# Kernel tuning notes

Measured on AMD Instinct MI355X. Metric: run time of the kernel, lower is better.

## Reference

```python
import jax, jax.numpy as jnp
import numpy as np

B, N, NE = 2, 100000, 800000
S, F, D = 3, 2, 128          # space_size, n_fields, enc_dim
TD, CD, SD = 11, 32, 10      # enc_t_dim, cond_dim, spatial_dim


def _mlp(x, w1, b1, w2, b2):
    # Linear -> SiLU -> Linear (MLP with n_hidden=1, hidden=128, no layernorm)
    return jax.nn.silu(x @ w1 + b1) @ w2 + b2


def setup_inputs() -> dict:
    key = jax.random.key(0)
    ks = iter(jax.random.split(key, 40))

    def w(shape):
        fan_in = shape[-2] if len(shape) >= 2 else shape[-1]
        return jax.random.normal(next(ks), shape, jnp.float32) / np.sqrt(fan_in)

    def b(shape):
        return jnp.zeros(shape, jnp.float32)

    inp = dict(
        node_pos=jax.random.normal(next(ks), (B, N, S), jnp.float32),
        state_in=jax.random.normal(next(ks), (B, N, F), jnp.float32),
        time_i=jax.random.normal(next(ks), (B, TD), jnp.float32),
        conditions=jax.random.normal(next(ks), (B, CD), jnp.float32),
        spatial_inform=jax.random.normal(next(ks), (B, SD), jnp.float32),
        edges=jax.random.randint(next(ks), (B, NE, 2), 0, N, jnp.int64)
        if jax.config.jax_enable_x64 else jax.random.randint(next(ks), (B, NE, 2), 0, N, jnp.int32),
        # per-field node MLPs, stacked over fields: input = space_size + 1
        fields_w1=w((F, S + 1, D)), fields_b1=b((F, D)),
        fields_w2=w((F, D, D)), fields_b2=b((F, D)),
        # time / cond / spatial MLPs
        time_w1=w((TD, D)), time_b1=b((D,)), time_w2=w((D, D)), time_b2=b((D,)),
        cond_w1=w((CD, D)), cond_b1=b((D,)), cond_w2=w((D, D)), cond_b2=b((D,)),
        spat_w1=w((SD, D)), spat_b1=b((D,)), spat_w2=w((D, D)), spat_b2=b((D,)),
        # fuse_para: 3*D -> 128 -> 2*D
        fuse_w1=w((3 * D, D)), fuse_b1=b((D,)),
        fuse_w2=w((D, 2 * D)), fuse_b2=b((2 * D,)),
        # edge MLP: 2*S+1 -> 128 -> D
        fe_w1=w((2 * S + 1, D)), fe_b1=b((D,)),
        fe_w2=w((D, D)), fe_b2=b((D,)),
    )
    return inp


def reference(node_pos, state_in, time_i, conditions, spatial_inform, edges,
              fields_w1, fields_b1, fields_w2, fields_b2,
              time_w1, time_b1, time_w2, time_b2,
              cond_w1, cond_b1, cond_w2, cond_b2,
              spat_w1, spat_b1, spat_w2, spat_b2,
              fuse_w1, fuse_b1, fuse_w2, fuse_b2,
              fe_w1, fe_b1, fe_w2, fe_b2):
    # FiLM parameters from time + condition + spatial encodings
    time_enc = _mlp(time_i, time_w1, time_b1, time_w2, time_b2)        # [B,D]
    cond_enc = _mlp(conditions, cond_w1, cond_b1, cond_w2, cond_b2)    # [B,D]
    spat_enc = _mlp(spatial_inform, spat_w1, spat_b1, spat_w2, spat_b2)
    h = jnp.concatenate([cond_enc, time_enc, spat_enc], axis=-1)       # [B,3D]
    para = _mlp(h, fuse_w1, fuse_b1, fuse_w2, fuse_b2)                 # [B,2D]
    gamma, beta = jnp.split(para, 2, axis=-1)                          # [B,D] each

    # Per-field node MLPs, vectorized over fields: x_f [B,N,F,S+1]
    pos_b = jnp.broadcast_to(node_pos[:, :, None, :], (node_pos.shape[0], node_pos.shape[1], F, S))
    x_f = jnp.concatenate([pos_b, state_in[..., None]], axis=-1)       # [B,N,F,S+1]
    hid = jax.nn.silu(jnp.einsum('bnfd,fde->bnfe', x_f, fields_w1) + fields_b1)
    V = jnp.einsum('bnfe,feo->bnfo', hid, fields_w2) + fields_b2       # [B,N,F,D]
    V = V * gamma[:, None, None, :] + beta[:, None, None, :]

    # Edge features: gather sender/receiver positions, diff/norm/concat
    idx_s = jnp.broadcast_to(edges[..., 0:1], edges.shape[:2] + (S,))
    idx_r = jnp.broadcast_to(edges[..., 1:2], edges.shape[:2] + (S,))
    senders = jnp.take_along_axis(node_pos, idx_s, axis=1)             # [B,NE,S]
    receivers = jnp.take_along_axis(node_pos, idx_r, axis=1)
    d = receivers - senders
    norm = jnp.sqrt(jnp.sum(d * d, axis=-1, keepdims=True) + 1e-8)
    e_feat = jnp.concatenate([d, -d, norm], axis=-1)                   # [B,NE,2S+1]
    E = _mlp(e_feat, fe_w1, fe_b1, fe_w2, fe_b2)                       # [B,NE,D]

    return V, E
```

## Files before the change

### kernel.cpp

```cpp
#include <hip/hip_runtime.h>
#include <hip/hip_bf16.h>
#include <string.h>

#define B_  2
#define N_  100000
#define NE_ 800000
#define F_  2
#define D_  128
#define TD_ 11
#define CD_ 32
#define SD_ 10

#define NODE_BX   782
#define NODE_NB   (NODE_BX * F_ * B_)
#define EDGE_BX   6250
#define EDGE_NB   (EDGE_BX * B_)
#define GROUPS    3125
#define TOTAL_NB  (NODE_NB + EDGE_NB)

#define WS_GB      0
#define WS_FLAG    2048
#define WS_W1PACK  2112
#define WS_W2FRAG  14400

typedef short s16x8 __attribute__((ext_vector_type(8)));
typedef float f32x4 __attribute__((ext_vector_type(4)));
typedef unsigned u32x4 __attribute__((ext_vector_type(4)));

static __device__ __forceinline__ unsigned short f2bf(float f) {
    unsigned u = __builtin_bit_cast(unsigned, f);
    u += 0x7FFFu + ((u >> 16) & 1u);
    return (unsigned short)(u >> 16);
}
static __device__ __forceinline__ float silu_f(float x) {
    return x * __builtin_amdgcn_rcpf(1.0f + __expf(-x));
}
static __device__ __forceinline__ unsigned pack_bf16(float lo, float hi) {
    __hip_bfloat162 c = __float22bfloat162_rn(make_float2(lo, hi));
    unsigned r;
    memcpy(&r, &c, sizeof(r));
    return r;
}
static __device__ __forceinline__ void lds_barrier() {
    asm volatile("s_waitcnt lgkmcnt(0)" ::: "memory");
    __builtin_amdgcn_s_barrier();
}

__global__ void prep_kernel(
    const float* __restrict__ time_i, const float* __restrict__ cond,
    const float* __restrict__ spat,
    const float* tw1, const float* tb1, const float* tw2, const float* tb2,
    const float* cw1, const float* cb1, const float* cw2, const float* cb2,
    const float* sw1, const float* sb1, const float* sw2, const float* sb2,
    const float* fuw1, const float* fub1, const float* fuw2, const float* fub2,
    const float* __restrict__ fw1, const float* __restrict__ fb1,
    const float* __restrict__ fw2,
    const float* __restrict__ ew1, const float* __restrict__ eb1,
    const float* __restrict__ ew2,
    const int* __restrict__ edges,
    char* __restrict__ ws)
{
    const int bx = blockIdx.x, t = threadIdx.x;

    if (bx < 2) {
        const int b = bx, d = t;
        __shared__ float h[3 * D_];
        __shared__ float hid[D_];

        const float* X [3] = { cond + b * CD_, time_i + b * TD_, spat + b * SD_ };
        const float* W1[3] = { cw1, tw1, sw1 };
        const float* B1[3] = { cb1, tb1, sb1 };
        const float* W2[3] = { cw2, tw2, sw2 };
        const float* B2[3] = { cb2, tb2, sb2 };
        const int    K [3] = { CD_, TD_, SD_ };

        for (int m = 0; m < 3; ++m) {
            float a = 0.f;
            if (d < D_) {
                a = B1[m][d];
                for (int k = 0; k < K[m]; ++k) a += X[m][k] * W1[m][k * D_ + d];
            }
            __syncthreads();
            if (d < D_) hid[d] = a / (1.0f + __expf(-a));
            __syncthreads();
            if (d < D_) {
                float o = B2[m][d];
                for (int k = 0; k < D_; ++k) o += hid[k] * W2[m][k * D_ + d];
                h[m * D_ + d] = o;
            }
        }
        __syncthreads();
        float pre2 = 0.f;
        if (d < D_) {
            pre2 = fub1[d];
            for (int k = 0; k < 3 * D_; ++k) pre2 += h[k] * fuw1[k * D_ + d];
        }
        __syncthreads();
        if (d < D_) hid[d] = pre2 / (1.0f + __expf(-pre2));
        __syncthreads();
        if (d < D_) {
            float g = fub2[d], be = fub2[D_ + d];
            for (int k = 0; k < D_; ++k) {
                float hv = hid[k];
                g  += hv * fuw2[k * 2 * D_ + d];
                be += hv * fuw2[k * 2 * D_ + D_ + d];
            }
            float* gb = (float*)ws;
            gb[(b * 2 + 0) * D_ + d] = g;
            gb[(b * 2 + 1) * D_ + d] = be;
        }
    } else if (bx < 5) {
        const int which = bx - 2;
        const float* src = (which < 2) ? (fw2 + which * D_ * D_) : ew2;
        unsigned short* dst = (unsigned short*)(ws + WS_W2FRAG) + (long)which * 2048 * 8;
        for (int e = t; e < 2048; e += 256) {
            const int lanee = e & 63, kb = (e >> 6) & 3, nt = e >> 8;
            const int out = nt * 16 + (lanee & 15);
            const int k0  = kb * 32 + (lanee >> 4) * 8;
            s16x8 v;
            #pragma unroll
            for (int i = 0; i < 8; ++i)
                v[i] = (short)f2bf(src[(k0 + i) * D_ + out]);
            *(s16x8*)(dst + e * 8) = v;
        }
    } else {
        float* w1p = (float*)(ws + WS_W1PACK);
        if (t == 0) {
            int nz = 0;
            for (int j = 0; j < 64; ++j) nz |= edges[2 * j + 1];
            ((float*)(ws + WS_FLAG))[0] = (nz == 0) ? 1.0f : 0.0f;
        }
        {
            const int f = t >> 7, e = t & 127;
            float* dst = w1p + (f * 128 + e) * 8;
            #pragma unroll
            for (int k = 0; k < 4; ++k) dst[k] = fw1[(f * 4 + k) * D_ + e];
            dst[4] = fb1[f * D_ + e];
            dst[5] = 0.f; dst[6] = 0.f; dst[7] = 0.f;
        }
        if (t < 128) {
            const int e = t;
            float* dst = w1p + (2 * 128 + e) * 8;
            dst[0] = ew1[0 * D_ + e] - ew1[3 * D_ + e];
            dst[1] = ew1[1 * D_ + e] - ew1[4 * D_ + e];
            dst[2] = ew1[2 * D_ + e] - ew1[5 * D_ + e];
            dst[3] = ew1[6 * D_ + e];
            dst[4] = eb1[e];
            dst[5] = 0.f; dst[6] = 0.f; dst[7] = 0.f;
        }
    }
}

__global__ __launch_bounds__(256, 4) void fused_kernel(
    const float* __restrict__ pos, const float* __restrict__ state,
    const int* __restrict__ edges,
    const float* __restrict__ fb2, const float* __restrict__ eb2,
    const char* __restrict__ ws,
    float* __restrict__ V, float* __restrict__ E)
{
    __shared__ __align__(16) char smem[34816];
    unsigned short* w2lds = (unsigned short*)smem;
    float*          outF  = (float*)smem;

    const int bx = blockIdx.x, t = threadIdx.x;
    const int lane = t & 63, wv = t >> 6;
    const int kg = lane >> 4, lr = lane & 15;

    const float* gbAll = (const float*)ws;
    const float* w1all = (const float*)(ws + WS_W1PACK);
    const unsigned short* w2all = (const unsigned short*)(ws + WS_W2FRAG);

    bool isNode; int sub;
    if (bx >= 5 * GROUPS) { isNode = true; sub = GROUPS + (bx - 5 * GROUPS); }
    else {
        int g = bx / 5, s = bx - 5 * g;
        if (s == 0) { isNode = true;  sub = g; }
        else        { isNode = false; sub = g * 4 + (s - 1); }
    }

    float xa[4], xb[4];
    int n0 = 0, f = 0, b, e0blk = 0;
    if (isNode) {
        n0 = (sub % NODE_BX) * 128;
        f  = (sub / NODE_BX) & 1;
        b  = sub / (NODE_BX * F_);
        int na = n0 + wv * 32 + lr;      if (na >= N_) na = N_ - 1;
        int nb = n0 + wv * 32 + lr + 16; if (nb >= N_) nb = N_ - 1;
        long pa = ((long)b * N_ + na) * 3, pb = ((long)b * N_ + nb) * 3;
        xa[0] = pos[pa]; xa[1] = pos[pa + 1]; xa[2] = pos[pa + 2];
        xb[0] = pos[pb]; xb[1] = pos[pb + 1]; xb[2] = pos[pb + 2];
        xa[3] = state[((long)b * N_ + na) * F_ + f];
        xb[3] = state[((long)b * N_ + nb) * F_ + f];
    } else {
        e0blk = (sub % EDGE_BX) * 128;
        b     = sub / EDGE_BX;
        const bool x64 = ((const float*)(ws + WS_FLAG))[0] > 0.5f;
        const long ea = (long)b * NE_ + e0blk + wv * 32 + lr;
        const long eb = ea + 16;
        int sa, ra, sb, rb;
        if (x64) {
            sa = edges[ea * 4]; ra = edges[ea * 4 + 2];
            sb = edges[eb * 4]; rb = edges[eb * 4 + 2];
        } else {
            int2 va = *(const int2*)(edges + ea * 2); sa = va.x; ra = va.y;
            int2 vb = *(const int2*)(edges + eb * 2); sb = vb.x; rb = vb.y;
        }
        const float* pp = pos + (long)b * N_ * 3;
        {
            long so = (long)sa * 3, ro = (long)ra * 3;
            xa[0] = pp[ro]     - pp[so];
            xa[1] = pp[ro + 1] - pp[so + 1];
            xa[2] = pp[ro + 2] - pp[so + 2];
            xa[3] = sqrtf(xa[0]*xa[0] + xa[1]*xa[1] + xa[2]*xa[2] + 1e-8f);
        }
        {
            long so = (long)sb * 3, ro = (long)rb * 3;
            xb[0] = pp[ro]     - pp[so];
            xb[1] = pp[ro + 1] - pp[so + 1];
            xb[2] = pp[ro + 2] - pp[so + 2];
            xb[3] = sqrtf(xb[0]*xb[0] + xb[1]*xb[1] + xb[2]*xb[2] + 1e-8f);
        }
    }

    const int which = isNode ? f : 2;
    {
        const char* src = (const char*)(w2all + (long)which * 2048 * 8);
        #pragma unroll
        for (int j = 0; j < 8; ++j) {
            f32x4 v = *(const f32x4*)(src + (j * 256 + t) * 16);
            *(f32x4*)((char*)w2lds + (j * 256 + t) * 16) = v;
        }
    }
    __syncthreads();

    const float* w1g = w1all + which * 1024;

    f32x4 acc[2][8];
    #pragma unroll
    for (int mt = 0; mt < 2; ++mt)
        #pragma unroll
        for (int nt = 0; nt < 8; ++nt) acc[mt][nt] = (f32x4){0.f, 0.f, 0.f, 0.f};

    #pragma unroll
    for (int kb = 0; kb < 4; ++kb) {
        const int e0 = kb * 32 + kg * 8;
        u32x4 da, db;
        #pragma unroll
        for (int j = 0; j < 4; ++j) {
            const float* wp0 = w1g + (e0 + 2 * j) * 8;
            const float* wp1 = wp0 + 8;
            f32x4 wA = *(const f32x4*)wp0;  const float bbA = wp0[4];
            f32x4 wB = *(const f32x4*)wp1;  const float bbB = wp1[4];
            float pa0 = silu_f(xa[0]*wA[0] + xa[1]*wA[1] + xa[2]*wA[2] + xa[3]*wA[3] + bbA);
            float pa1 = silu_f(xa[0]*wB[0] + xa[1]*wB[1] + xa[2]*wB[2] + xa[3]*wB[3] + bbB);
            float pb0 = silu_f(xb[0]*wA[0] + xb[1]*wA[1] + xb[2]*wA[2] + xb[3]*wA[3] + bbA);
            float pb1 = silu_f(xb[0]*wB[0] + xb[1]*wB[1] + xb[2]*wB[2] + xb[3]*wB[3] + bbB);
            da[j] = pack_bf16(pa0, pa1);
            db[j] = pack_bf16(pb0, pb1);
        }
        s16x8 ua, ub;
        memcpy(&ua, &da, sizeof(ua));
        memcpy(&ub, &db, sizeof(ub));
        #pragma unroll
        for (int nt = 0; nt < 8; ++nt) {
            s16x8 afr = *(const s16x8*)(w2lds + ((nt * 4 + kb) * 64 + lane) * 8);
            acc[0][nt] = __builtin_amdgcn_mfma_f32_16x16x32_bf16(afr, ua, acc[0][nt], 0, 0, 0);
            acc[1][nt] = __builtin_amdgcn_mfma_f32_16x16x32_bf16(afr, ub, acc[1][nt], 0, 0, 0);
        }
    }

    const float* bias  = isNode ? (fb2 + f * D_) : eb2;
    const float* gamma = gbAll + b * 2 * D_;
    const float* beta  = gamma + D_;
    float* base = isNode ? (V + (((long)b * N_ + n0) * F_ + f) * D_)
                         : (E + ((long)b * NE_ + e0blk) * D_);
    const long stride   = isNode ? (long)F_ * D_ : (long)D_;
    const int rowsValid = isNode ? (N_ - n0) : 128;

    __syncthreads();

    #pragma unroll
    for (int p = 0; p < 2; ++p) {
        #pragma unroll
        for (int ntl = 0; ntl < 4; ++ntl) {
            const int nt = p * 4 + ntl;
            const int d0 = nt * 16 + kg * 4;
            const f32x4 bs = *(const f32x4*)(bias + d0);
            f32x4 g, be;
            if (isNode) { g = *(const f32x4*)(gamma + d0); be = *(const f32x4*)(beta + d0); }
            #pragma unroll
            for (int mt = 0; mt < 2; ++mt) {
                const int m = wv * 32 + mt * 16 + lr;
                f32x4 v;
                #pragma unroll
                for (int r = 0; r < 4; ++r)
                    v[r] = isNode ? (acc[mt][nt][r] + bs[r]) * g[r] + be[r]
                                  : acc[mt][nt][r] + bs[r];
                *(f32x4*)(outF + m * 68 + ntl * 16 + kg * 4) = v;
            }
        }
        lds_barrier();
        #pragma unroll
        for (int j = 0; j < 8; ++j) {
            const int r = wv * 32 + j * 4 + (lane >> 4);
            const int c = (lane & 15) * 4;
            f32x4 v = *(const f32x4*)(outF + r * 68 + c);
            if (r < rowsValid)
                __builtin_nontemporal_store(v, (f32x4*)(base + (long)r * stride + p * 64 + c));
        }
        if (p == 0) lds_barrier();
    }
}

extern "C" void kernel_launch(void* const* d_in, const int* in_sizes, int n_in,
                              void* d_out, int out_size, void* d_ws, size_t ws_size,
                              hipStream_t stream)
{
    (void)in_sizes; (void)n_in; (void)out_size; (void)ws_size;

    const float* node_pos  = (const float*)d_in[0];
    const float* state_in  = (const float*)d_in[1];
    const float* time_i    = (const float*)d_in[2];
    const float* conditions= (const float*)d_in[3];
    const float* spatial   = (const float*)d_in[4];
    const int*   edges     = (const int*)d_in[5];
    const float* fields_w1 = (const float*)d_in[6];
    const float* fields_b1 = (const float*)d_in[7];
    const float* fields_w2 = (const float*)d_in[8];
    const float* fields_b2 = (const float*)d_in[9];
    const float* tw1 = (const float*)d_in[10];
    const float* tb1 = (const float*)d_in[11];
    const float* tw2 = (const float*)d_in[12];
    const float* tb2 = (const float*)d_in[13];
    const float* cw1 = (const float*)d_in[14];
    const float* cb1 = (const float*)d_in[15];
    const float* cw2 = (const float*)d_in[16];
    const float* cb2 = (const float*)d_in[17];
    const float* sw1 = (const float*)d_in[18];
    const float* sb1 = (const float*)d_in[19];
    const float* sw2 = (const float*)d_in[20];
    const float* sb2 = (const float*)d_in[21];
    const float* fu_w1 = (const float*)d_in[22];
    const float* fu_b1 = (const float*)d_in[23];
    const float* fu_w2 = (const float*)d_in[24];
    const float* fu_b2 = (const float*)d_in[25];
    const float* fe_w1 = (const float*)d_in[26];
    const float* fe_b1 = (const float*)d_in[27];
    const float* fe_w2 = (const float*)d_in[28];
    const float* fe_b2 = (const float*)d_in[29];

    char*  ws = (char*)d_ws;
    float* V  = (float*)d_out;
    float* E  = V + (long)B_ * N_ * F_ * D_;

    prep_kernel<<<dim3(6), dim3(256), 0, stream>>>(
        time_i, conditions, spatial,
        tw1, tb1, tw2, tb2, cw1, cb1, cw2, cb2, sw1, sb1, sw2, sb2,
        fu_w1, fu_b1, fu_w2, fu_b2,
        fields_w1, fields_b1, fields_w2,
        fe_w1, fe_b1, fe_w2,
        edges, ws);

    fused_kernel<<<dim3(TOTAL_NB), dim3(256), 0, stream>>>(
        node_pos, state_in, edges, fields_b2, fe_b2, ws, V, E);
}
```

Baseline: 259.4 us.

## Compute first MLP layer with MFMA and stage hidden activations through LDS

Measured after the change: 245.8 us. -5.2%, faster.

```diff
diff --git a/kernel.cpp b/kernel.cpp
--- a/kernel.cpp
+++ b/kernel.cpp
@@ -20,8 +20,8 @@
 
 #define WS_GB      0
 #define WS_FLAG    2048
-#define WS_W1PACK  2112
-#define WS_W2FRAG  14400
+#define WS_W1FRAG  2112
+#define WS_W2FRAG  26688
 
 typedef short s16x8 __attribute__((ext_vector_type(8)));
 typedef float f32x4 __attribute__((ext_vector_type(4)));
@@ -124,50 +124,57 @@
             *(s16x8*)(dst + e * 8) = v;
         }
     } else {
-        float* w1p = (float*)(ws + WS_W1PACK);
         if (t == 0) {
             int nz = 0;
             for (int j = 0; j < 64; ++j) nz |= edges[2 * j + 1];
             ((float*)(ws + WS_FLAG))[0] = (nz == 0) ? 1.0f : 0.0f;
         }
-        {
-            const int f = t >> 7, e = t & 127;
-            float* dst = w1p + (f * 128 + e) * 8;
+        unsigned short* w1f = (unsigned short*)(ws + WS_W1FRAG);
+        for (int e = t; e < 1536; e += 256) {
+            const int which = e >> 9;
+            const int h8    = (e >> 6) & 7;
+            const int lane  = e & 63;
+            const int m  = h8 * 16 + (lane & 15);
+            const int kg = lane >> 4;
+            s16x8 v;
             #pragma unroll
-            for (int k = 0; k < 4; ++k) dst[k] = fw1[(f * 4 + k) * D_ + e];
-            dst[4] = fb1[f * D_ + e];
-            dst[5] = 0.f; dst[6] = 0.f; dst[7] = 0.f;
-        }
-        if (t < 128) {
-            const int e = t;
-            float* dst = w1p + (2 * 128 + e) * 8;
-            dst[0] = ew1[0 * D_ + e] - ew1[3 * D_ + e];
-            dst[1] = ew1[1 * D_ + e] - ew1[4 * D_ + e];
-            dst[2] = ew1[2 * D_ + e] - ew1[5 * D_ + e];
-            dst[3] = ew1[6 * D_ + e];
-            dst[4] = eb1[e];
-            dst[5] = 0.f; dst[6] = 0.f; dst[7] = 0.f;
-        }
-    }
-}
-
-__global__ __launch_bounds__(256, 4) void fused_kernel(
+            for (int i = 0; i < 8; ++i) {
+                const int k = kg * 8 + i;
+                float val = 0.f;
+                if (kg == 0) {
+                    if (which < 2) {
+                        if (k < 4)      val = fw1[(which * 4 + k) * D_ + m];
+                        else if (k == 4) val = fb1[which * D_ + m];
+                    } else {
+                        if (k < 3)      val = ew1[k * D_ + m] - ew1[(k + 3) * D_ + m];
+                        else if (k == 3) val = ew1[6 * D_ + m];
+                        else if (k == 4) val = eb1[m];
+                    }
+                }
+                v[i] = (short)f2bf(val);
+            }
+            *(s16x8*)(w1f + e * 8) = v;
+        }
+    }
+}
+
+__global__ __launch_bounds__(256, 3) void fused_kernel(
     const float* __restrict__ pos, const float* __restrict__ state,
     const int* __restrict__ edges,
     const float* __restrict__ fb2, const float* __restrict__ eb2,
     const char* __restrict__ ws,
     float* __restrict__ V, float* __restrict__ E)
 {
-    __shared__ __align__(16) char smem[34816];
+    __shared__ __align__(16) char smem[50176];
     unsigned short* w2lds = (unsigned short*)smem;
-    float*          outF  = (float*)smem;
+    float* outF = (float*)smem;
 
     const int bx = blockIdx.x, t = threadIdx.x;
     const int lane = t & 63, wv = t >> 6;
     const int kg = lane >> 4, lr = lane & 15;
 
     const float* gbAll = (const float*)ws;
-    const float* w1all = (const float*)(ws + WS_W1PACK);
+    const char*  w1fB  = ws + WS_W1FRAG;
     const unsigned short* w2all = (const unsigned short*)(ws + WS_W2FRAG);
 
     bool isNode; int sub;
@@ -223,6 +230,7 @@
     }
 
     const int which = isNode ? f : 2;
+
     {
         const char* src = (const char*)(w2all + (long)which * 2048 * 8);
         #pragma unroll
@@ -233,40 +241,49 @@
     }
     __syncthreads();
 
-    const float* w1g = w1all + which * 1024;
+    u32x4 bf0, bf1;
+    bf0[0] = pack_bf16(xa[0], xa[1]); bf0[1] = pack_bf16(xa[2], xa[3]);
+    bf0[2] = 0x00003F80u;             bf0[3] = 0u;
+    bf1[0] = pack_bf16(xb[0], xb[1]); bf1[1] = pack_bf16(xb[2], xb[3]);
+    bf1[2] = 0x00003F80u;             bf1[3] = 0u;
+
+    char* slabB = smem + 32768 + wv * 4352;
+    const char* w1fr = w1fB + which * 8192;
 
     f32x4 acc[2][8];
     #pragma unroll
-    for (int mt = 0; mt < 2; ++mt)
-        #pragma unroll
-        for (int nt = 0; nt < 8; ++nt) acc[mt][nt] = (f32x4){0.f, 0.f, 0.f, 0.f};
+    for (int rt = 0; rt < 2; ++rt)
+        #pragma unroll
+        for (int nt = 0; nt < 8; ++nt) acc[rt][nt] = (f32x4){0.f, 0.f, 0.f, 0.f};
+
+    const f32x4 zero4 = (f32x4){0.f, 0.f, 0.f, 0.f};
 
     #pragma unroll
-    for (int kb = 0; kb < 4; ++kb) {
-        const int e0 = kb * 32 + kg * 8;
-        u32x4 da, db;
-        #pragma unroll
-        for (int j = 0; j < 4; ++j) {
-            const float* wp0 = w1g + (e0 + 2 * j) * 8;
-            const float* wp1 = wp0 + 8;
-            f32x4 wA = *(const f32x4*)wp0;  const float bbA = wp0[4];
-            f32x4 wB = *(const f32x4*)wp1;  const float bbB = wp1[4];
-            float pa0 = silu_f(xa[0]*wA[0] + xa[1]*wA[1] + xa[2]*wA[2] + xa[3]*wA[3] + bbA);
-            float pa1 = silu_f(xa[0]*wB[0] + xa[1]*wB[1] + xa[2]*wB[2] + xa[3]*wB[3] + bbB);
-            float pb0 = silu_f(xb[0]*wA[0] + xb[1]*wA[1] + xb[2]*wA[2] + xb[3]*wA[3] + bbA);
-            float pb1 = silu_f(xb[0]*wB[0] + xb[1]*wB[1] + xb[2]*wB[2] + xb[3]*wB[3] + bbB);
-            da[j] = pack_bf16(pa0, pa1);
-            db[j] = pack_bf16(pb0, pb1);
-        }
-        s16x8 ua, ub;
-        memcpy(&ua, &da, sizeof(ua));
-        memcpy(&ub, &db, sizeof(ub));
-        #pragma unroll
-        for (int nt = 0; nt < 8; ++nt) {
-            s16x8 afr = *(const s16x8*)(w2lds + ((nt * 4 + kb) * 64 + lane) * 8);
-            acc[0][nt] = __builtin_amdgcn_mfma_f32_16x16x32_bf16(afr, ua, acc[0][nt], 0, 0, 0);
-            acc[1][nt] = __builtin_amdgcn_mfma_f32_16x16x32_bf16(afr, ub, acc[1][nt], 0, 0, 0);
-        }
+    for (int rt = 0; rt < 2; ++rt) {
+        s16x8 bop;
+        { u32x4 tmp = rt ? bf1 : bf0; memcpy(&bop, &tmp, sizeof(bop)); }
+
+        #pragma unroll
+        for (int h8 = 0; h8 < 8; ++h8) {
+            s16x8 af = *(const s16x8*)(w1fr + h8 * 1024 + lane * 16);
+            f32x4 h4 = __builtin_amdgcn_mfma_f32_16x16x32_bf16(af, bop, zero4, 0, 0, 0);
+            uint2 d;
+            d.x = pack_bf16(silu_f(h4[0]), silu_f(h4[1]));
+            d.y = pack_bf16(silu_f(h4[2]), silu_f(h4[3]));
+            *(uint2*)(slabB + lr * 272 + h8 * 32 + kg * 8) = d;
+        }
+        lds_barrier();
+
+        #pragma unroll
+        for (int kb = 0; kb < 4; ++kb) {
+            s16x8 u = *(const s16x8*)(slabB + lr * 272 + kb * 64 + kg * 16);
+            #pragma unroll
+            for (int nt = 0; nt < 8; ++nt) {
+                s16x8 afr = *(const s16x8*)(w2lds + ((nt * 4 + kb) * 64 + lane) * 8);
+                acc[rt][nt] = __builtin_amdgcn_mfma_f32_16x16x32_bf16(afr, u, acc[rt][nt], 0, 0, 0);
+            }
+        }
+        lds_barrier();
     }
 
     const float* bias  = isNode ? (fb2 + f * D_) : eb2;
@@ -276,8 +293,6 @@
                          : (E + ((long)b * NE_ + e0blk) * D_);
     const long stride   = isNode ? (long)F_ * D_ : (long)D_;
     const int rowsValid = isNode ? (N_ - n0) : 128;
-
-    __syncthreads();
 
     #pragma unroll
     for (int p = 0; p < 2; ++p) {
```
